# Kernel tuning notes

Hardware: AMD Instinct MI355X
Metric: run time of the kernel (lower is better)

Reference implementation:

```python
import jax, jax.numpy as jnp
import numpy as np

D_IN = 1024
D_OUT = 1024
NUM_HEADS = 16
D_HEAD = D_OUT // NUM_HEADS


def setup_inputs() -> dict:
    key = jax.random.key(0)
    ks = jax.random.split(key, 6)
    s = 0.02
    x = jax.random.normal(ks[0], (2, 2048, D_IN), dtype=jnp.float32)
    Wq = jax.random.normal(ks[1], (D_IN, D_OUT), dtype=jnp.float32) * s
    Wk = jax.random.normal(ks[2], (D_IN, D_OUT), dtype=jnp.float32) * s
    Wv = jax.random.normal(ks[3], (D_IN, D_OUT), dtype=jnp.float32) * s
    Wo = jax.random.normal(ks[4], (D_OUT, D_OUT), dtype=jnp.float32) * s
    bo = jnp.zeros((D_OUT,), dtype=jnp.float32)
    return {"x": x, "Wq": Wq, "Wk": Wk, "Wv": Wv, "Wo": Wo, "bo": bo}


def reference(x, Wq, Wk, Wv, Wo, bo):
    bs, S, _ = x.shape
    # QKV projections -> [b, h, s, d]
    def split_heads(t):
        return t.reshape(bs, S, NUM_HEADS, D_HEAD).transpose(0, 2, 1, 3)
    q = split_heads(x @ Wq)
    k = split_heads(x @ Wk)
    v = split_heads(x @ Wv)
    # scores [b, h, s, s], causal mask, scaled softmax
    scores = jnp.einsum("bhqd,bhkd->bhqk", q, k)
    causal = jnp.tril(jnp.ones((S, S), dtype=bool))
    scores = jnp.where(causal, scores, -jnp.inf)
    attn = jax.nn.softmax(scores / jnp.sqrt(jnp.float32(D_HEAD)), axis=-1)
    # dropout rate is 0.0 -> identity
    ctx = jnp.einsum("bhqk,bhkd->bhqd", attn, v)
    ctx = ctx.transpose(0, 2, 1, 3).reshape(bs, S, D_OUT)
    return ctx @ Wo + bo
```

## Files before the change

kernel.cpp:

```cpp
#include <hip/hip_runtime.h>
#include <math.h>

namespace {

constexpr int S   = 2048;
constexpr int D   = 1024;
constexpr int H   = 16;
constexpr int DH  = 64;
constexpr int B   = 2;
constexpr int M   = B * S;

typedef __attribute__((ext_vector_type(8)))  short bf16x8;
typedef __attribute__((ext_vector_type(4)))  float f32x4;
typedef __attribute__((ext_vector_type(16))) float f32x16;

__device__ __forceinline__ unsigned short f2bf(float f) {
    unsigned u = __builtin_bit_cast(unsigned, f);
    u += 0x7fffu + ((u >> 16) & 1u);
    return (unsigned short)(u >> 16);
}

__device__ __forceinline__ unsigned cvt_pk_bf16(float lo, float hi) {
    unsigned r;
    asm("v_cvt_pk_bf16_f32 %0, %1, %2" : "=v"(r) : "v"(lo), "v"(hi));
    return r;
}

__device__ __forceinline__ void gload16(const void* g, void* l) {
    __builtin_amdgcn_global_load_lds(
        (const __attribute__((address_space(1))) void*)g,
        (__attribute__((address_space(3))) void*)l, 16, 0, 0);
}

__global__ __launch_bounds__(256) void convert_x(
    const float* __restrict__ x, unsigned short* __restrict__ xb)
{
    const int i = (blockIdx.x * 256 + threadIdx.x) * 8;
    float4 a = *(const float4*)&x[i];
    float4 b = *(const float4*)&x[i + 4];
    ushort4 lo, hi;
    lo.x = f2bf(a.x); lo.y = f2bf(a.y); lo.z = f2bf(a.z); lo.w = f2bf(a.w);
    hi.x = f2bf(b.x); hi.y = f2bf(b.y); hi.z = f2bf(b.z); hi.w = f2bf(b.w);
    *(ushort4*)&xb[i]     = lo;
    *(ushort4*)&xb[i + 4] = hi;
}

__global__ __launch_bounds__(64) void convert_w(
    const float* __restrict__ Wq, const float* __restrict__ Wk,
    const float* __restrict__ Wv, const float* __restrict__ Wo,
    unsigned short* __restrict__ Wt)
{
    const int mat = blockIdx.z;
    const float* W = (mat == 0) ? Wq : (mat == 1) ? Wk : (mat == 2) ? Wv : Wo;
    const int n  = blockIdx.y * 64 + threadIdx.x;
    const int k0 = blockIdx.x * 8;
    ushort4 u0, u1;
    u0.x = f2bf(W[(size_t)(k0 + 0) * D + n]);
    u0.y = f2bf(W[(size_t)(k0 + 1) * D + n]);
    u0.z = f2bf(W[(size_t)(k0 + 2) * D + n]);
    u0.w = f2bf(W[(size_t)(k0 + 3) * D + n]);
    u1.x = f2bf(W[(size_t)(k0 + 4) * D + n]);
    u1.y = f2bf(W[(size_t)(k0 + 5) * D + n]);
    u1.z = f2bf(W[(size_t)(k0 + 6) * D + n]);
    u1.w = f2bf(W[(size_t)(k0 + 7) * D + n]);
    unsigned short* o = Wt + (size_t)mat * D * D + (size_t)n * D + k0;
    *(ushort4*)&o[0] = u0;
    *(ushort4*)&o[4] = u1;
}

__global__ __launch_bounds__(256) void gemm_qkv(
    const unsigned short* __restrict__ xb, const unsigned short* __restrict__ Wt,
    unsigned short* __restrict__ Qb, unsigned short* __restrict__ Kb,
    unsigned short* __restrict__ Vt)
{
    __shared__ unsigned short As0[128 * 32];
    __shared__ unsigned short As1[128 * 32];
    __shared__ unsigned short Bs0[128 * 32];
    __shared__ unsigned short Bs1[128 * 32];

    const int tid = threadIdx.x;
    const int l  = tid & 63;
    const int w  = tid >> 6;
    const int lr = l & 15;
    const int g  = l >> 4;
    const int wr = w >> 1, wc = w & 1;

    const int bm  = blockIdx.y;
    const int bnl = blockIdx.x;
    const int mat = bnl >> 3;
    const int n0  = (bnl & 7) * 128;
    const int m0  = bm * 128;
    const unsigned short* Bp = Wt + (size_t)mat * D * D;

    const int lrow = l >> 2;
    const int lcol = (l & 3) * 8;

    f32x4 acc[4][4];
    #pragma unroll
    for (int i = 0; i < 4; ++i)
        #pragma unroll
        for (int j = 0; j < 4; ++j) acc[i][j] = (f32x4){0.f, 0.f, 0.f, 0.f};

#define QKV_STAGE(AD, BD, kk0)                                                    \
    {                                                                             \
        _Pragma("unroll")                                                         \
        for (int p = 0; p < 2; ++p) {                                             \
            const int c = w * 2 + p;                                              \
            gload16(&xb[(size_t)(m0 + c * 16 + lrow) * D + (kk0) + lcol],         \
                    &AD[c * 512]);                                                \
            gload16(&Bp[(size_t)(n0 + c * 16 + lrow) * D + (kk0) + lcol],         \
                    &BD[c * 512]);                                                \
        }                                                                         \
    }

#define QKV_COMP(AS, BS)                                                          \
    {                                                                             \
        bf16x8 af[4], bfr[4];                                                     \
        _Pragma("unroll")                                                         \
        for (int i = 0; i < 4; ++i) {                                             \
            af[i]  = *(const bf16x8*)&AS[(wr * 64 + i * 16 + lr) * 32 + g * 8];   \
            bfr[i] = *(const bf16x8*)&BS[(wc * 64 + i * 16 + lr) * 32 + g * 8];   \
        }                                                                         \
        _Pragma("unroll")                                                         \
        for (int mi = 0; mi < 4; ++mi)                                            \
            _Pragma("unroll")                                                     \
            for (int ni = 0; ni < 4; ++ni)                                        \
                acc[mi][ni] = __builtin_amdgcn_mfma_f32_16x16x32_bf16(            \
                    af[mi], bfr[ni], acc[mi][ni], 0, 0, 0);                       \
    }

    QKV_STAGE(As0, Bs0, 0);
    __syncthreads();
    for (int k0 = 0; k0 < D; k0 += 64) {
        QKV_STAGE(As1, Bs1, k0 + 32);
        QKV_COMP(As0, Bs0);
        __syncthreads();
        if (k0 + 64 < D) QKV_STAGE(As0, Bs0, k0 + 64);
        QKV_COMP(As1, Bs1);
        __syncthreads();
    }
#undef QKV_STAGE
#undef QKV_COMP

    const int b      = m0 >> 11;
    const int s_base = (m0 & (S - 1)) + wr * 64;
    if (mat == 2) {
        #pragma unroll
        for (int ni = 0; ni < 4; ++ni) {
            const int n  = n0 + wc * 64 + ni * 16 + lr;
            const int bh = b * H + (n >> 6);
            unsigned short* vp = Vt + ((size_t)bh * DH + (n & 63)) * S;
            #pragma unroll
            for (int mi = 0; mi < 4; ++mi) {
                const int s0 = s_base + mi * 16 + g * 4;
                ushort4 u;
                u.x = f2bf(acc[mi][ni][0]); u.y = f2bf(acc[mi][ni][1]);
                u.z = f2bf(acc[mi][ni][2]); u.w = f2bf(acc[mi][ni][3]);
                *(ushort4*)&vp[s0] = u;
            }
        }
    } else {
        unsigned short* Op = (mat == 0) ? Qb : Kb;
        #pragma unroll
        for (int mi = 0; mi < 4; ++mi)
            #pragma unroll
            for (int r = 0; r < 4; ++r) {
                const int s = s_base + mi * 16 + g * 4 + r;
                #pragma unroll
                for (int ni = 0; ni < 4; ++ni) {
                    const int n  = n0 + wc * 64 + ni * 16 + lr;
                    const int bh = b * H + (n >> 6);
                    Op[((size_t)bh * S + s) * DH + (n & 63)] = f2bf(acc[mi][ni][r]);
                }
            }
    }
}

__global__ __launch_bounds__(256) void gemm_out(
    const unsigned short* __restrict__ ctxb, const unsigned short* __restrict__ Wot,
    const float* __restrict__ bo, float* __restrict__ out)
{
    __shared__ unsigned short As[64 * 32];
    __shared__ unsigned short Bs[128 * 32];

    const int tid = threadIdx.x;
    const int l  = tid & 63;
    const int w  = tid >> 6;
    const int lr = l & 15;
    const int g  = l >> 4;
    const int wr = w >> 1, wc = w & 1;

    const int m0 = blockIdx.y * 64;
    const int n0 = blockIdx.x * 128;

    const int lrow = l >> 2;
    const int lcol = (l & 3) * 8;

    f32x4 acc[2][4];
    #pragma unroll
    for (int i = 0; i < 2; ++i)
        #pragma unroll
        for (int j = 0; j < 4; ++j) acc[i][j] = (f32x4){0.f, 0.f, 0.f, 0.f};

    for (int k0 = 0; k0 < D; k0 += 32) {
        gload16(&ctxb[(size_t)(m0 + w * 16 + lrow) * D + k0 + lcol], &As[w * 512]);
        #pragma unroll
        for (int p = 0; p < 2; ++p) {
            const int c = w * 2 + p;
            gload16(&Wot[(size_t)(n0 + c * 16 + lrow) * D + k0 + lcol], &Bs[c * 512]);
        }
        __syncthreads();
        bf16x8 af[2], bfr[4];
        #pragma unroll
        for (int i = 0; i < 2; ++i)
            af[i] = *(const bf16x8*)&As[(wr * 32 + i * 16 + lr) * 32 + g * 8];
        #pragma unroll
        for (int i = 0; i < 4; ++i)
            bfr[i] = *(const bf16x8*)&Bs[(wc * 64 + i * 16 + lr) * 32 + g * 8];
        #pragma unroll
        for (int mi = 0; mi < 2; ++mi)
            #pragma unroll
            for (int ni = 0; ni < 4; ++ni)
                acc[mi][ni] = __builtin_amdgcn_mfma_f32_16x16x32_bf16(
                    af[mi], bfr[ni], acc[mi][ni], 0, 0, 0);
        __syncthreads();
    }

    #pragma unroll
    for (int mi = 0; mi < 2; ++mi)
        #pragma unroll
        for (int ni = 0; ni < 4; ++ni) {
            const int n = n0 + wc * 64 + ni * 16 + lr;
            const float bias = bo[n];
            #pragma unroll
            for (int r = 0; r < 4; ++r) {
                const int m = m0 + wr * 32 + mi * 16 + g * 4 + r;
                out[(size_t)m * D + n] = acc[mi][ni][r] + bias;
            }
        }
}

__global__ __launch_bounds__(256, 2) void attn_mfma32(
    const unsigned short* __restrict__ Qb, const unsigned short* __restrict__ Kb,
    const unsigned short* __restrict__ Vt, unsigned short* __restrict__ ctxb)
{
    __shared__ unsigned short Ks0[64 * 64];
    __shared__ unsigned short Ks1[64 * 64];
    __shared__ unsigned short Vs0[64 * 64];
    __shared__ unsigned short Vs1[64 * 64];

    const int tid = threadIdx.x;
    const int l   = tid & 63;
    const int w   = tid >> 6;
    const int l31 = l & 31;
    const int hi  = l >> 5;

    const int lid = blockIdx.x;
    const int xcd = lid & 7;
    const int jj  = lid >> 3;
    const int rnd = jj >> 5;
    const int pos = jj & 31;
    const int sub = pos >> 4;
    const int k16 = pos & 15;
    const int bh  = xcd * 4 + rnd * 2 + sub;
    const int qt  = rnd ? k16 : 15 - k16;
    const int q0w = qt * 128 + w * 32;
    const int Fw  = q0w >> 6;
    const int NT  = 2 * qt + 2;

    const unsigned short* Qp = Qb + (size_t)bh * S * DH;
    const unsigned short* Kp = Kb + (size_t)bh * S * DH;
    const unsigned short* Vp = Vt + (size_t)bh * DH * S;

    bf16x8 qf[4];
    #pragma unroll
    for (int kk = 0; kk < 4; ++kk)
        qf[kk] = *(const bf16x8*)&Qp[(size_t)(q0w + l31) * DH + kk * 16 + hi * 8];

    f32x16 acc0 = {}, acc1 = {};
    float m = -1e30f, ll = 0.f;

    const int srow = l >> 3;
    const int ssw  = 8 * ((l & 7) ^ srow);

#define ATTN_STAGE(KD, VD, t)                                                 \
    {                                                                         \
        const int kv0s = (t) * 64;                                            \
        _Pragma("unroll")                                                     \
        for (int p = 0; p < 2; ++p) {                                         \
            const int c   = w * 2 + p;                                        \
            const int row = c * 8 + srow;                                     \
            gload16(Kp + (size_t)(kv0s + row) * DH + ssw, &KD[c * 512]);      \
            gload16(Vp + (size_t)row * S + kv0s + ssw, &VD[c * 512]);         \
        }                                                                     \
    }

#define ATTN_STEP(KSB, VSB, TT)                                               \
    if ((TT) <= Fw) {                                                         \
        const int kv0  = (TT) * 64;                                           \
        const bool diag = ((TT) == Fw);                                       \
        f32x16 stl = {}, sth = {};                                            \
        _Pragma("unroll")                                                     \
        for (int kk = 0; kk < 4; ++kk) {                                      \
            const int cc = kk * 2 + hi;                                       \
            bf16x8 kl = *(const bf16x8*)&KSB[l31 * 64 + ((cc ^ (l31 & 7)) * 8)]; \
            bf16x8 kh = *(const bf16x8*)&KSB[(32 + l31) * 64 + ((cc ^ (l31 & 7)) * 8)]; \
            stl = __builtin_amdgcn_mfma_f32_32x32x16_bf16(kl, qf[kk], stl, 0, 0, 0); \
            sth = __builtin_amdgcn_mfma_f32_32x32x16_bf16(kh, qf[kk], sth, 0, 0, 0); \
        }                                                                     \
        const int qg = q0w + l31;                                             \
        float sc0[16], sc1[16];                                               \
        float pmax = -3e38f;                                                  \
        _Pragma("unroll")                                                     \
        for (int r = 0; r < 16; ++r) {                                        \
            const int koff = (r & 3) + 8 * (r >> 2) + 4 * hi;                 \
            float a = stl[r] * 0.125f;                                        \
            float b2 = sth[r] * 0.125f;                                       \
            if (diag) {                                                       \
                if (kv0 + koff > qg)      a  = -3e38f;                        \
                if (kv0 + 32 + koff > qg) b2 = -3e38f;                        \
            }                                                                 \
            sc0[r] = a; sc1[r] = b2;                                          \
            pmax = fmaxf(pmax, fmaxf(a, b2));                                 \
        }                                                                     \
        pmax = fmaxf(pmax, __shfl_xor(pmax, 32));                             \
        if (!__all(pmax <= m + 8.f)) {                                        \
            const float newm = fmaxf(m, pmax);                                \
            const float corr = __expf(m - newm);                              \
            ll *= corr;                                                       \
            _Pragma("unroll")                                                 \
            for (int r = 0; r < 16; ++r) { acc0[r] *= corr; acc1[r] *= corr; }\
            m = newm;                                                         \
        }                                                                     \
        float p0[16], p1[16], psum = 0.f;                                     \
        _Pragma("unroll")                                                     \
        for (int r = 0; r < 16; ++r) {                                        \
            p0[r] = __expf(sc0[r] - m); psum += p0[r];                        \
            p1[r] = __expf(sc1[r] - m); psum += p1[r];                        \
        }                                                                     \
        ll += psum + __shfl_xor(psum, 32);                                    \
        unsigned pw[16];                                                      \
        _Pragma("unroll")                                                     \
        for (int tt = 0; tt < 8; ++tt) {                                      \
            pw[tt]     = cvt_pk_bf16(p0[2 * tt], p0[2 * tt + 1]);             \
            pw[8 + tt] = cvt_pk_bf16(p1[2 * tt], p1[2 * tt + 1]);             \
        }                                                                     \
        __builtin_amdgcn_s_setprio(1);                                        \
        _Pragma("unroll")                                                     \
        for (int ck = 0; ck < 4; ++ck) {                                      \
            const int t00 = 2 * ((2 * ck) & 3) + 8 * (ck >> 1);               \
            const int t10 = 2 * ((2 * ck + 1) & 3) + 8 * (ck >> 1);           \
            const unsigned sw0 = hi ? pw[t10]     : pw[t00];                  \
            const unsigned sw1 = hi ? pw[t10 + 1] : pw[t00 + 1];              \
            const unsigned e0i = hi ? pw[t00]     : pw[t10];                  \
            const unsigned e1i = hi ? pw[t00 + 1] : pw[t10 + 1];              \
            const unsigned e0  = __shfl_xor(e0i, 32);                         \
            const unsigned e1  = __shfl_xor(e1i, 32);                         \
            union { unsigned u[4]; bf16x8 v; } pb;                            \
            pb.u[0] = hi ? e0  : sw0;                                         \
            pb.u[1] = hi ? e1  : sw1;                                         \
            pb.u[2] = hi ? sw0 : e0;                                          \
            pb.u[3] = hi ? sw1 : e1;                                          \
            const int cc = ck * 2 + hi;                                       \
            bf16x8 v0 = *(const bf16x8*)&VSB[l31 * 64 + ((cc ^ (l31 & 7)) * 8)]; \
            bf16x8 v1 = *(const bf16x8*)&VSB[(32 + l31) * 64 + ((cc ^ (l31 & 7)) * 8)]; \
            acc0 = __builtin_amdgcn_mfma_f32_32x32x16_bf16(v0, pb.v, acc0, 0, 0, 0); \
            acc1 = __builtin_amdgcn_mfma_f32_32x32x16_bf16(v1, pb.v, acc1, 0, 0, 0); \
        }                                                                     \
        __builtin_amdgcn_s_setprio(0);                                        \
    }

    ATTN_STAGE(Ks0, Vs0, 0);
    __syncthreads();

    for (int t = 0; t < NT; t += 2) {
        ATTN_STAGE(Ks1, Vs1, t + 1);
        ATTN_STEP(Ks0, Vs0, t);
        __syncthreads();
        if (t + 2 < NT) ATTN_STAGE(Ks0, Vs0, t + 2);
        ATTN_STEP(Ks1, Vs1, t + 1);
        __syncthreads();
    }
#undef ATTN_STAGE
#undef ATTN_STEP

    const float inv = 1.f / ll;
    const int bb = bh >> 4, hh = bh & (H - 1);
    const int q  = q0w + l31;
    unsigned short* op = ctxb + ((size_t)(bb * S + q)) * D + hh * DH;
    #pragma unroll
    for (int t = 0; t < 8; ++t) {
        const int r0 = 2 * t;
        const int d  = (r0 & 3) + 8 * (r0 >> 2) + 4 * hi;
        *(unsigned*)&op[d]      = cvt_pk_bf16(acc0[r0] * inv, acc0[r0 + 1] * inv);
        *(unsigned*)&op[32 + d] = cvt_pk_bf16(acc1[r0] * inv, acc1[r0 + 1] * inv);
    }
}

}

extern "C" void kernel_launch(void* const* d_in, const int* in_sizes, int n_in,
                              void* d_out, int out_size, void* d_ws, size_t ws_size,
                              hipStream_t stream) {
    const float* x  = (const float*)d_in[0];
    const float* Wq = (const float*)d_in[1];
    const float* Wk = (const float*)d_in[2];
    const float* Wv = (const float*)d_in[3];
    const float* Wo = (const float*)d_in[4];
    const float* bo = (const float*)d_in[5];
    float* out = (float*)d_out;

    unsigned short* xb   = (unsigned short*)d_ws;
    unsigned short* Wt   = xb + (size_t)M * D;
    unsigned short* Qb   = Wt + (size_t)4 * D * D;
    unsigned short* Kb   = Qb + (size_t)M * D;
    unsigned short* Vtp  = Kb + (size_t)M * D;
    unsigned short* ctxb = Vtp + (size_t)M * D;

    convert_x<<<dim3((M * D) / (256 * 8)), 256, 0, stream>>>(x, xb);
    convert_w<<<dim3(D / 8, D / 64, 4), 64, 0, stream>>>(Wq, Wk, Wv, Wo, Wt);
    gemm_qkv<<<dim3(24, M / 128), 256, 0, stream>>>(xb, Wt, Qb, Kb, Vtp);
    attn_mfma32<<<dim3(512), 256, 0, stream>>>(Qb, Kb, Vtp, ctxb);
    gemm_out<<<dim3(D / 128, M / 64), 256, 0, stream>>>(
        ctxb, Wt + (size_t)3 * D * D, bo, out);
}
```

Baseline: 205.6 us.

## Split attention KV range across two wave groups and double-buffer output GEMM

The attention kernel now uses 512-thread blocks, where two groups of four waves each process half of the causal KV range for the same query tile. The two partial results are merged through shared memory with a log-sum-exp rescale, and each block handles a balanced pair of query tiles, so the grid shrinks from 512 blocks to 256. Separately, the output projection GEMM gets double-buffered LDS staging, so the next K-slice load overlaps the current MFMA work. The costs are extra shared memory, extra barriers for the merge, and fewer blocks in flight.

```diff
diff --git a/kernel.cpp b/kernel.cpp
--- a/kernel.cpp
+++ b/kernel.cpp
@@ -180,8 +180,10 @@
     const unsigned short* __restrict__ ctxb, const unsigned short* __restrict__ Wot,
     const float* __restrict__ bo, float* __restrict__ out)
 {
-    __shared__ unsigned short As[64 * 32];
-    __shared__ unsigned short Bs[128 * 32];
+    __shared__ unsigned short As0[64 * 32];
+    __shared__ unsigned short As1[64 * 32];
+    __shared__ unsigned short Bs0[128 * 32];
+    __shared__ unsigned short Bs1[128 * 32];
 
     const int tid = threadIdx.x;
     const int l  = tid & 63;
@@ -202,29 +204,47 @@
         #pragma unroll
         for (int j = 0; j < 4; ++j) acc[i][j] = (f32x4){0.f, 0.f, 0.f, 0.f};
 
-    for (int k0 = 0; k0 < D; k0 += 32) {
-        gload16(&ctxb[(size_t)(m0 + w * 16 + lrow) * D + k0 + lcol], &As[w * 512]);
-        #pragma unroll
-        for (int p = 0; p < 2; ++p) {
-            const int c = w * 2 + p;
-            gload16(&Wot[(size_t)(n0 + c * 16 + lrow) * D + k0 + lcol], &Bs[c * 512]);
-        }
-        __syncthreads();
-        bf16x8 af[2], bfr[4];
-        #pragma unroll
-        for (int i = 0; i < 2; ++i)
-            af[i] = *(const bf16x8*)&As[(wr * 32 + i * 16 + lr) * 32 + g * 8];
-        #pragma unroll
-        for (int i = 0; i < 4; ++i)
-            bfr[i] = *(const bf16x8*)&Bs[(wc * 64 + i * 16 + lr) * 32 + g * 8];
-        #pragma unroll
-        for (int mi = 0; mi < 2; ++mi)
-            #pragma unroll
-            for (int ni = 0; ni < 4; ++ni)
-                acc[mi][ni] = __builtin_amdgcn_mfma_f32_16x16x32_bf16(
-                    af[mi], bfr[ni], acc[mi][ni], 0, 0, 0);
-        __syncthreads();
-    }
+#define OUT_STAGE(AD, BD, kk0)                                                    \
+    {                                                                             \
+        gload16(&ctxb[(size_t)(m0 + w * 16 + lrow) * D + (kk0) + lcol],           \
+                &AD[w * 512]);                                                    \
+        _Pragma("unroll")                                                         \
+        for (int p = 0; p < 2; ++p) {                                             \
+            const int c = w * 2 + p;                                              \
+            gload16(&Wot[(size_t)(n0 + c * 16 + lrow) * D + (kk0) + lcol],        \
+                    &BD[c * 512]);                                                \
+        }                                                                         \
+    }
+
+#define OUT_COMP(AS, BS)                                                          \
+    {                                                                             \
+        bf16x8 af[2], bfr[4];                                                     \
+        _Pragma("unroll")                                                         \
+        for (int i = 0; i < 2; ++i)                                               \
+            af[i] = *(const bf16x8*)&AS[(wr * 32 + i * 16 + lr) * 32 + g * 8];    \
+        _Pragma("unroll")                                                         \
+        for (int i = 0; i < 4; ++i)                                               \
+            bfr[i] = *(const bf16x8*)&BS[(wc * 64 + i * 16 + lr) * 32 + g * 8];   \
+        _Pragma("unroll")                                                         \
+        for (int mi = 0; mi < 2; ++mi)                                            \
+            _Pragma("unroll")                                                     \
+            for (int ni = 0; ni < 4; ++ni)                                        \
+                acc[mi][ni] = __builtin_amdgcn_mfma_f32_16x16x32_bf16(            \
+                    af[mi], bfr[ni], acc[mi][ni], 0, 0, 0);                       \
+    }
+
+    OUT_STAGE(As0, Bs0, 0);
+    __syncthreads();
+    for (int k0 = 0; k0 < D; k0 += 64) {
+        OUT_STAGE(As1, Bs1, k0 + 32);
+        OUT_COMP(As0, Bs0);
+        __syncthreads();
+        if (k0 + 64 < D) OUT_STAGE(As0, Bs0, k0 + 64);
+        OUT_COMP(As1, Bs1);
+        __syncthreads();
+    }
+#undef OUT_STAGE
+#undef OUT_COMP
 
     #pragma unroll
     for (int mi = 0; mi < 2; ++mi)
@@ -240,55 +260,17 @@
         }
 }
 
-__global__ __launch_bounds__(256, 2) void attn_mfma32(
-    const unsigned short* __restrict__ Qb, const unsigned short* __restrict__ Kb,
-    const unsigned short* __restrict__ Vt, unsigned short* __restrict__ ctxb)
-{
-    __shared__ unsigned short Ks0[64 * 64];
-    __shared__ unsigned short Ks1[64 * 64];
-    __shared__ unsigned short Vs0[64 * 64];
-    __shared__ unsigned short Vs1[64 * 64];
-
-    const int tid = threadIdx.x;
-    const int l   = tid & 63;
-    const int w   = tid >> 6;
-    const int l31 = l & 31;
-    const int hi  = l >> 5;
-
-    const int lid = blockIdx.x;
-    const int xcd = lid & 7;
-    const int jj  = lid >> 3;
-    const int rnd = jj >> 5;
-    const int pos = jj & 31;
-    const int sub = pos >> 4;
-    const int k16 = pos & 15;
-    const int bh  = xcd * 4 + rnd * 2 + sub;
-    const int qt  = rnd ? k16 : 15 - k16;
-    const int q0w = qt * 128 + w * 32;
-    const int Fw  = q0w >> 6;
-    const int NT  = 2 * qt + 2;
-
-    const unsigned short* Qp = Qb + (size_t)bh * S * DH;
-    const unsigned short* Kp = Kb + (size_t)bh * S * DH;
-    const unsigned short* Vp = Vt + (size_t)bh * DH * S;
-
-    bf16x8 qf[4];
-    #pragma unroll
-    for (int kk = 0; kk < 4; ++kk)
-        qf[kk] = *(const bf16x8*)&Qp[(size_t)(q0w + l31) * DH + kk * 16 + hi * 8];
-
-    f32x16 acc0 = {}, acc1 = {};
-    float m = -1e30f, ll = 0.f;
-
-    const int srow = l >> 3;
-    const int ssw  = 8 * ((l & 7) ^ srow);
-
-#define ATTN_STAGE(KD, VD, t)                                                 \
+union AttnShared {
+    unsigned short stage[8][4096];
+    float mrg[4][64][34];
+};
+
+#define ATTN_STAGE(KD, VD, TT)                                                \
     {                                                                         \
-        const int kv0s = (t) * 64;                                            \
+        const int kv0s = (TT) * 64;                                           \
         _Pragma("unroll")                                                     \
         for (int p = 0; p < 2; ++p) {                                         \
-            const int c   = w * 2 + p;                                        \
+            const int c   = wq * 2 + p;                                       \
             const int row = c * 8 + srow;                                     \
             gload16(Kp + (size_t)(kv0s + row) * DH + ssw, &KD[c * 512]);      \
             gload16(Vp + (size_t)row * S + kv0s + ssw, &VD[c * 512]);         \
@@ -370,32 +352,114 @@
         __builtin_amdgcn_s_setprio(0);                                        \
     }
 
-    ATTN_STAGE(Ks0, Vs0, 0);
-    __syncthreads();
-
-    for (int t = 0; t < NT; t += 2) {
-        ATTN_STAGE(Ks1, Vs1, t + 1);
-        ATTN_STEP(Ks0, Vs0, t);
-        __syncthreads();
-        if (t + 2 < NT) ATTN_STAGE(Ks0, Vs0, t + 2);
-        ATTN_STEP(Ks1, Vs1, t + 1);
-        __syncthreads();
-    }
+template<int HALF>
+__device__ __forceinline__ void attn_side(
+    const unsigned short* __restrict__ Qp, const unsigned short* __restrict__ Kp,
+    const unsigned short* __restrict__ Vp, unsigned short* __restrict__ opb,
+    AttnShared& sh, int jpair, int wq, int l, int l31, int hi, int srow, int ssw)
+{
+    unsigned short* const K0 = sh.stage[HALF * 4 + 0];
+    unsigned short* const V0 = sh.stage[HALF * 4 + 1];
+    unsigned short* const K1 = sh.stage[HALF * 4 + 2];
+    unsigned short* const V1 = sh.stage[HALF * 4 + 3];
+
+    for (int it = 0; it < 2; ++it) {
+        const int qt    = it ? jpair : 15 - jpair;
+        const int hB    = qt + 1;
+        const int steps = qt + 1;
+        const int tb0   = HALF ? hB : 0;
+        const int q0w   = qt * 128 + wq * 32;
+        const int Fw    = q0w >> 6;
+
+        bf16x8 qf[4];
+        #pragma unroll
+        for (int kk = 0; kk < 4; ++kk)
+            qf[kk] = *(const bf16x8*)&Qp[(size_t)(q0w + l31) * DH + kk * 16 + hi * 8];
+
+        f32x16 acc0 = {}, acc1 = {};
+        float m = -1e30f, ll = 0.f;
+
+        ATTN_STAGE(K0, V0, tb0);
+        __syncthreads();
+        int i = 0;
+        while (i + 2 <= steps) {
+            ATTN_STAGE(K1, V1, tb0 + i + 1);
+            ATTN_STEP(K0, V0, tb0 + i);
+            __syncthreads();
+            if (i + 2 < steps) ATTN_STAGE(K0, V0, tb0 + i + 2);
+            ATTN_STEP(K1, V1, tb0 + i + 1);
+            __syncthreads();
+            i += 2;
+        }
+        if (i < steps) {
+            ATTN_STEP(K0, V0, tb0 + i);
+            __syncthreads();
+        }
+
+        if (HALF == 0) {
+            float* mb = sh.mrg[wq][l];
+            #pragma unroll
+            for (int r = 0; r < 16; ++r) { mb[r] = acc0[r]; mb[16 + r] = acc1[r]; }
+            mb[32] = m; mb[33] = ll;
+        }
+        __syncthreads();
+        if (HALF == 1) {
+            const float* mb = sh.mrg[wq][l];
+            const float mA = mb[32], lA = mb[33];
+            const float ms = fmaxf(m, mA);
+            const float cB = __expf(m - ms);
+            const float cA = __expf(mA - ms);
+            const float inv = 1.f / (ll * cB + lA * cA);
+            unsigned short* op = opb + (size_t)(q0w + l31) * D;
+            #pragma unroll
+            for (int t = 0; t < 8; ++t) {
+                const int r0 = 2 * t, r1 = 2 * t + 1;
+                const int d  = (r0 & 3) + 8 * (r0 >> 2) + 4 * hi;
+                const float a0 = (acc0[r0] * cB + mb[r0]      * cA) * inv;
+                const float a1 = (acc0[r1] * cB + mb[r1]      * cA) * inv;
+                const float b0 = (acc1[r0] * cB + mb[16 + r0] * cA) * inv;
+                const float b1 = (acc1[r1] * cB + mb[16 + r1] * cA) * inv;
+                *(unsigned*)&op[d]      = cvt_pk_bf16(a0, a1);
+                *(unsigned*)&op[32 + d] = cvt_pk_bf16(b0, b1);
+            }
+        }
+        __syncthreads();
+    }
+}
+
+__global__ __launch_bounds__(512, 2) void attn_mfma32(
+    const unsigned short* __restrict__ Qb, const unsigned short* __restrict__ Kb,
+    const unsigned short* __restrict__ Vt, unsigned short* __restrict__ ctxb)
+{
+    __shared__ AttnShared sh;
+
+    const int tid = threadIdx.x;
+    const int l   = tid & 63;
+    const int w   = tid >> 6;
+    const int wq  = w & 3;
+    const int l31 = l & 31;
+    const int hi  = l >> 5;
+    const int srow = l >> 3;
+    const int ssw  = 8 * ((l & 7) ^ srow);
+
+    const int bid = blockIdx.x;
+    const int xcd = bid & 7;
+    const int u   = bid >> 3;
+    const int bh  = xcd * 4 + (u >> 3);
+    const int jpair = u & 7;
+
+    const unsigned short* Qp = Qb + (size_t)bh * S * DH;
+    const unsigned short* Kp = Kb + (size_t)bh * S * DH;
+    const unsigned short* Vp = Vt + (size_t)bh * DH * S;
+    const int bb = bh >> 4, hh = bh & (H - 1);
+    unsigned short* opb = ctxb + (size_t)bb * S * D + hh * DH;
+
+    if (w < 4) attn_side<0>(Qp, Kp, Vp, opb, sh, jpair, wq, l, l31, hi, srow, ssw);
+    else       attn_side<1>(Qp, Kp, Vp, opb, sh, jpair, wq, l, l31, hi, srow, ssw);
+}
+
 #undef ATTN_STAGE
 #undef ATTN_STEP
-
-    const float inv = 1.f / ll;
-    const int bb = bh >> 4, hh = bh & (H - 1);
-    const int q  = q0w + l31;
-    unsigned short* op = ctxb + ((size_t)(bb * S + q)) * D + hh * DH;
-    #pragma unroll
-    for (int t = 0; t < 8; ++t) {
-        const int r0 = 2 * t;
-        const int d  = (r0 & 3) + 8 * (r0 >> 2) + 4 * hi;
-        *(unsigned*)&op[d]      = cvt_pk_bf16(acc0[r0] * inv, acc0[r0 + 1] * inv);
-        *(unsigned*)&op[32 + d] = cvt_pk_bf16(acc1[r0] * inv, acc1[r0 + 1] * inv);
-    }
-}
 
 }
 
@@ -420,7 +484,7 @@
     convert_x<<<dim3((M * D) / (256 * 8)), 256, 0, stream>>>(x, xb);
     convert_w<<<dim3(D / 8, D / 64, 4), 64, 0, stream>>>(Wq, Wk, Wv, Wo, Wt);
     gemm_qkv<<<dim3(24, M / 128), 256, 0, stream>>>(xb, Wt, Qb, Kb, Vtp);
-    attn_mfma32<<<dim3(512), 256, 0, stream>>>(Qb, Kb, Vtp, ctxb);
+    attn_mfma32<<<dim3(256), 512, 0, stream>>>(Qb, Kb, Vtp, ctxb);
     gemm_out<<<dim3(D / 128, M / 64), 256, 0, stream>>>(
         ctxb, Wt + (size_t)3 * D * D, bo, out);
 }
```

Result: faster. 194.0 us (-5.6%).
